# Optimization experiments

Hardware: AMD Instinct MI355X
Metric: run time of the kernel (lower is better)

Reference implementation:

```python
import jax, jax.numpy as jnp
import numpy as np

N = 8192
IN_F = 256
HID = 192
OUT_F = 3


def setup_inputs() -> dict:
    key = jax.random.key(0)
    ks = jax.random.split(key, 8)
    features = jax.random.normal(ks[0], (N, IN_F), dtype=jnp.float32)
    # dense (row-stochastic-ish) adjacency; sparse pattern scaled to keep magnitudes sane
    adj = (jax.random.uniform(ks[1], (N, N), dtype=jnp.float32) < (32.0 / N)).astype(jnp.float32) / 32.0
    def winit(k, shape):
        stdv = 0.6 * 6.0 / np.sqrt(shape[0] + shape[1])
        return jax.random.uniform(k, shape, jnp.float32, -stdv, stdv)
    W1 = winit(ks[2], (IN_F, HID))
    b1 = jax.random.uniform(ks[3], (HID,), jnp.float32, -0.1, 0.1)
    W_mid = jnp.stack([winit(jax.random.fold_in(ks[4], i), (HID, HID)) for i in range(12)])
    b_mid = jax.random.uniform(ks[5], (12, HID), jnp.float32, -0.1, 0.1)
    W_out = winit(ks[6], (HID, OUT_F))
    b_out = jax.random.uniform(ks[7], (OUT_F,), jnp.float32, -0.1, 0.1)
    return dict(features=features, adj=adj, W1=W1, b1=b1,
                W_mid=W_mid, b_mid=b_mid, W_out=W_out, b_out=b_out)


def zngcn(x, adj, W, b):
    # support = x @ W; first side_len cols aggregated over adj, rest passed through
    support = x @ W
    side_len = max(W.shape[1] // 3, 2)
    side_1 = adj @ support[:, :side_len]   # [N, side_len]
    out = jnp.concatenate([side_1, support[:, side_len:]], axis=1)
    return out + b


def reference(features, adj, W1, b1, W_mid, b_mid, W_out, b_out):
    relu = jax.nn.relu
    x = relu(zngcn(features, adj, W1, b1))            # gc1
    x = relu(zngcn(x, adj, W_mid[0], b_mid[0]))       # gc2
    feat = (features[:, :HID] + x) * 0.5
    # gc3..gc12 as 5 residual pairs (W_mid indices 1..10)
    for i in (1, 3, 5, 7, 9):
        x = relu(zngcn(feat, adj, W_mid[i], b_mid[i]))
        x = relu(zngcn(x, adj, W_mid[i + 1], b_mid[i + 1]))
        feat = (feat + x) * 0.5
    # gc13 single layer (W_mid index 11)
    x = relu(zngcn(feat, adj, W_mid[11], b_mid[11]))
    feat = (feat + x) * 0.5
    coords = zngcn(feat, adj, W_out, b_out)           # gc14
    return coords, feat
```

## Files before the change

### kernel.cpp

```cpp
#include <hip/hip_runtime.h>
#include <hip/hip_bf16.h>

#define N_NODES 8192
#define CAP 128
#define XSTR 200
#define FFSTR 193
#define NBLK 512
#define SUPSZ (N_NODES * 64)
#define LEAF_BASE 16384

typedef short s16x8 __attribute__((ext_vector_type(8)));
typedef float f32x4 __attribute__((ext_vector_type(4)));
typedef unsigned short u16x8 __attribute__((ext_vector_type(8)));

__device__ __forceinline__ void cstoref(float* p, float v) {
    __hip_atomic_store(p, v, __ATOMIC_RELAXED, __HIP_MEMORY_SCOPE_AGENT);
}
__device__ __forceinline__ void cstoreh(unsigned short* p, unsigned short v) {
    __hip_atomic_store(p, v, __ATOMIC_RELAXED, __HIP_MEMORY_SCOPE_AGENT);
}
__device__ __forceinline__ void cstorei(int* p, int v) {
    __hip_atomic_store(p, v, __ATOMIC_RELAXED, __HIP_MEMORY_SCOPE_AGENT);
}
__device__ __forceinline__ int cloadi(const int* p) {
    return __hip_atomic_load(p, __ATOMIC_RELAXED, __HIP_MEMORY_SCOPE_AGENT);
}
__device__ __forceinline__ float b2f(unsigned short u) {
    union { unsigned int i; float f; } c; c.i = ((unsigned int)u) << 16; return c.f;
}
__device__ __forceinline__ unsigned short f2b(float f) {
    return __bfloat16_as_ushort(__float2bfloat16(f));
}

__global__ __launch_bounds__(256) void prep(
    const unsigned int* __restrict__ adj,
    const float* __restrict__ W1, const float* __restrict__ Wm,
    int* __restrict__ cnt, int* __restrict__ cols,
    unsigned short* __restrict__ Wt1, unsigned short* __restrict__ WtM)
{
    const int tid = threadIdx.x;
    if (blockIdx.x >= 2048) {
        int idx = (int)(blockIdx.x - 2048) * 256 + tid;
        if (idx >= 6144 + 55296) return;
        const float* src; unsigned short* dst; int KT, t, c, lane;
        if (idx < 6144) {
            KT = 8; src = W1; dst = Wt1;
            t = idx / 512; c = (idx >> 6) & 7; lane = idx & 63;
        } else {
            int r = idx - 6144;
            int mat = r / 4608;
            int rem = r % 4608;
            KT = 6; src = Wm + (size_t)mat * 36864; dst = WtM + (size_t)mat * 36864;
            t = rem / 384; c = (rem >> 6) % 6; lane = rem & 63;
        }
        int n = t * 16 + (lane & 15);
        int k0 = c * 32 + ((lane >> 4) << 3);
        u16x8 o;
#pragma unroll
        for (int j = 0; j < 8; ++j)
            o[j] = f2b(src[(size_t)(k0 + j) * 192 + n]);
        *reinterpret_cast<u16x8*>(dst + ((size_t)(t * KT + c) * 64 + lane) * 8) = o;
        return;
    }

    __shared__ int cntL[4];
    __shared__ int colsL[4][CAP];
    const int wave = tid >> 6;
    const int lane = tid & 63;
    const int row = (int)blockIdx.x * 4 + wave;
    if (lane == 0) cntL[wave] = 0;
    __syncthreads();

    const unsigned int* arow = adj + ((size_t)row << 13);
    uint4 buf[2][8];
    auto loadb = [&](int b, uint4* v) {
#pragma unroll
        for (int i = 0; i < 8; ++i) {
            int chunk = (b * 8 + i) * 64 + lane;
            v[i] = *reinterpret_cast<const uint4*>(arow + ((size_t)chunk << 2));
        }
    };
    loadb(0, buf[0]);
    for (int b = 0; b < 4; ++b) {
        if (b < 3) loadb(b + 1, buf[(b + 1) & 1]);
        uint4* v = buf[b & 1];
#pragma unroll
        for (int i = 0; i < 8; ++i) {
            if ((v[i].x | v[i].y | v[i].z | v[i].w) == 0u) continue;
            int e0 = ((b * 8 + i) * 64 + lane) << 2;
            int loc[4]; int k = 0;
            if (v[i].x) loc[k++] = e0;
            if (v[i].y) loc[k++] = e0 + 1;
            if (v[i].z) loc[k++] = e0 + 2;
            if (v[i].w) loc[k++] = e0 + 3;
            int pos = atomicAdd(&cntL[wave], k);
            for (int j = 0; j < k; ++j)
                if (pos + j < CAP) colsL[wave][pos + j] = loc[j];
        }
    }
    __syncthreads();
    int n = cntL[wave]; if (n > CAP) n = CAP;
    if (lane == 0) cnt[row] = n;
    for (int j = lane; j < CAP; j += 64)
        cols[(size_t)row * CAP + j] = (j < n) ? colsL[wave][j] : 0;
}

__device__ __forceinline__ void gbar_arrive(int* bar, int phase) {
    asm volatile("s_waitcnt vmcnt(0)" ::: "memory");
    __syncthreads();
    if (threadIdx.x == 0)
        cstorei(bar + blockIdx.x * 32, phase);
}
__device__ __forceinline__ void gbar_wait(int* bar, int phase) {
    const int tid = threadIdx.x;
    if (tid < 64) {
        if ((blockIdx.x & 15) == 0) {
            const int leaf = blockIdx.x >> 4;
            int rounds = 0;
            for (;;) {
                int v = (tid < 16) ? cloadi(bar + (leaf * 16 + tid) * 32)
                                   : 0x7fffffff;
#pragma unroll
                for (int off = 32; off > 0; off >>= 1)
                    v = min(v, __shfl_xor(v, off));
                if (v >= phase) break;
                __builtin_amdgcn_s_sleep(1);
                if (++rounds > (1 << 20)) break;
            }
            if (tid == 0) cstorei(bar + LEAF_BASE + leaf * 32, phase);
        }
        int rounds = 0;
        for (;;) {
            int v = (tid < 32) ? cloadi(bar + LEAF_BASE + tid * 32)
                               : 0x7fffffff;
#pragma unroll
            for (int off = 32; off > 0; off >>= 1)
                v = min(v, __shfl_xor(v, off));
            if (v >= phase) break;
            if (rounds < 8) __builtin_amdgcn_s_sleep(1);
            else            __builtin_amdgcn_s_sleep(4);
            if (++rounds > (1 << 20)) break;
        }
    }
    __syncthreads();
}

template<int KT>
__device__ __forceinline__ void load_a(s16x8* a, const unsigned short* xs,
                                       int lane, int quad) {
    const short* xr = reinterpret_cast<const short*>(xs) + (lane & 15) * XSTR + quad * 8;
#pragma unroll
    for (int c = 0; c < KT; ++c) a[c] = *reinterpret_cast<const s16x8*>(xr + c * 32);
}

__device__ __forceinline__ void load_a_feat(s16x8* a, const float* __restrict__ features,
                                            int m0, int lane, int quad) {
    const float* fr = features + (((size_t)(m0 + (lane & 15))) << 8) + quad * 8;
#pragma unroll
    for (int c = 0; c < 8; ++c) {
        float4 f0 = *reinterpret_cast<const float4*>(fr + c * 32);
        float4 f1 = *reinterpret_cast<const float4*>(fr + c * 32 + 4);
        s16x8 v;
        v[0] = (short)f2b(f0.x); v[1] = (short)f2b(f0.y);
        v[2] = (short)f2b(f0.z); v[3] = (short)f2b(f0.w);
        v[4] = (short)f2b(f1.x); v[5] = (short)f2b(f1.y);
        v[6] = (short)f2b(f1.z); v[7] = (short)f2b(f1.w);
        a[c] = v;
    }
}

template<int EP>
__device__ __forceinline__ void pass_epilogue(
    const f32x4& acc, int n, const float* __restrict__ bias,
    unsigned short* xdst, float* featL,
    const float* __restrict__ featG, float* __restrict__ outFeat,
    int m0, int quad)
{
#pragma unroll
    for (int r = 0; r < 4; ++r) {
        const int m = quad * 4 + r;
        float v = acc[r] + bias[n];
        float x = fmaxf(v, 0.f);
        if constexpr (EP == 0) {
            xdst[m * XSTR + n] = f2b(x);
        } else if constexpr (EP == 1) {
            float f = (featG[(size_t)(m0 + m) * 256 + n] + x) * 0.5f;
            featL[m * FFSTR + n] = f;
            xdst[m * XSTR + n] = f2b(f);
        } else if constexpr (EP == 2) {
            float f = (featL[m * FFSTR + n] + x) * 0.5f;
            featL[m * FFSTR + n] = f;
            xdst[m * XSTR + n] = f2b(f);
        } else {
            float f = (featL[m * FFSTR + n] + x) * 0.5f;
            featL[m * FFSTR + n] = f;
            outFeat[(size_t)(m0 + m) * 192 + n] = f;
        }
    }
}

template<int EP>
__device__ __forceinline__ void agg_phase(
    const unsigned short* __restrict__ supR,
    const int* colsL, const int* cntL,
    const float* __restrict__ bias, unsigned short* xdst,
    float* featL, const float* __restrict__ featG,
    float* __restrict__ outFeat,
    int m0, int lane, int wave)
{
    const int base = wave * 4;
    int na[4];
#pragma unroll
    for (int rr = 0; rr < 4; ++rr) na[rr] = cntL[base + rr];
    int nmax = max(max(na[0], na[1]), max(na[2], na[3]));
    float s[4] = {0.f, 0.f, 0.f, 0.f};
    for (int k = 0; k < nmax; k += 8) {
        float v[32];
#pragma unroll
        for (int rr = 0; rr < 4; ++rr) {
            int4 c0 = *reinterpret_cast<const int4*>(colsL + (base + rr) * CAP + k);
            int4 c1 = *reinterpret_cast<const int4*>(colsL + (base + rr) * CAP + k + 4);
            v[rr * 8 + 0] = b2f(supR[((size_t)(c0.x & 8191) << 6) + lane]);
            v[rr * 8 + 1] = b2f(supR[((size_t)(c0.y & 8191) << 6) + lane]);
            v[rr * 8 + 2] = b2f(supR[((size_t)(c0.z & 8191) << 6) + lane]);
            v[rr * 8 + 3] = b2f(supR[((size_t)(c0.w & 8191) << 6) + lane]);
            v[rr * 8 + 4] = b2f(supR[((size_t)(c1.x & 8191) << 6) + lane]);
            v[rr * 8 + 5] = b2f(supR[((size_t)(c1.y & 8191) << 6) + lane]);
            v[rr * 8 + 6] = b2f(supR[((size_t)(c1.z & 8191) << 6) + lane]);
            v[rr * 8 + 7] = b2f(supR[((size_t)(c1.w & 8191) << 6) + lane]);
        }
#pragma unroll
        for (int rr = 0; rr < 4; ++rr) {
#pragma unroll
            for (int j = 0; j < 8; ++j)
                s[rr] += (k + j < na[rr]) ? v[rr * 8 + j] : 0.f;
        }
    }
#pragma unroll
    for (int rr = 0; rr < 4; ++rr) {
        const int lrow = base + rr;
        const int row = m0 + lrow;
        float vv = s[rr] * 0.03125f + bias[lane];
        float x = fmaxf(vv, 0.f);
        if constexpr (EP == 0) {
            xdst[lrow * XSTR + lane] = f2b(x);
        } else if constexpr (EP == 1) {
            float f = (featG[(size_t)row * 256 + lane] + x) * 0.5f;
            featL[lrow * FFSTR + lane] = f;
            xdst[lrow * XSTR + lane] = f2b(f);
        } else if constexpr (EP == 2) {
            float f = (featL[lrow * FFSTR + lane] + x) * 0.5f;
            featL[lrow * FFSTR + lane] = f;
            xdst[lrow * XSTR + lane] = f2b(f);
        } else {
            float f = (featL[lrow * FFSTR + lane] + x) * 0.5f;
            featL[lrow * FFSTR + lane] = f;
            outFeat[(size_t)row * 192 + lane] = f;
        }
    }
}

template<int EPprev, int EPcur>
__device__ __forceinline__ void layer_step(
    int* bar, int ph,
    unsigned short* xsPrev, unsigned short* xsCur,
    const unsigned short* __restrict__ supPrev, unsigned short* __restrict__ supCur,
    const unsigned short* __restrict__ Wt,
    const float* __restrict__ biasPrev, const float* __restrict__ biasCur,
    float* featL, const float* __restrict__ featG, float* __restrict__ outFeat,
    const int* colsL, const int* cntL,
    int m0, int lane, int wave, int quad)
{
    gbar_wait(bar, ph);
    agg_phase<EPprev>(supPrev, colsL, cntL, biasPrev, xsPrev, featL, featG,
                      outFeat, m0, lane, wave);
    __syncthreads();
    s16x8 a[6];
    load_a<6>(a, xsPrev, lane, quad);
    const short* wb = reinterpret_cast<const short*>(Wt);
    {
        f32x4 accS = {};
        const short* wp = wb + ((size_t)wave * 6 * 64 + lane) * 8;
#pragma unroll
        for (int c = 0; c < 6; ++c) {
            s16x8 b = *reinterpret_cast<const s16x8*>(wp + (size_t)c * 512);
            accS = __builtin_amdgcn_mfma_f32_16x16x32_bf16(a[c], b, accS, 0, 0, 0);
        }
        const int n = wave * 16 + (lane & 15);
#pragma unroll
        for (int r = 0; r < 4; ++r)
            cstoreh(&supCur[(((size_t)(m0 + quad * 4 + r)) << 6) + n], f2b(accS[r]));
    }
    gbar_arrive(bar, ph + 1);
#pragma unroll
    for (int p = 0; p < 2; ++p) {
        const int t = 4 + p * 4 + wave;
        f32x4 acc = {};
        const short* wp = wb + ((size_t)t * 6 * 64 + lane) * 8;
#pragma unroll
        for (int c = 0; c < 6; ++c) {
            s16x8 b = *reinterpret_cast<const s16x8*>(wp + (size_t)c * 512);
            acc = __builtin_amdgcn_mfma_f32_16x16x32_bf16(a[c], b, acc, 0, 0, 0);
        }
        const int n = t * 16 + (lane & 15);
        pass_epilogue<EPcur>(acc, n, biasCur, xsCur, featL, featG, outFeat, m0, quad);
    }
}

__global__ __launch_bounds__(256, 2) void fused_layers(
    const float* __restrict__ features,
    const int* __restrict__ cnt, const int* __restrict__ cols,
    const unsigned short* __restrict__ Wt1, const unsigned short* __restrict__ WtM,
    const float* __restrict__ b1, const float* __restrict__ bm,
    const float* __restrict__ Wout, const float* __restrict__ bout,
    unsigned short* __restrict__ supBase, float* __restrict__ sup3,
    float* __restrict__ out, float* __restrict__ outFeat,
    int* __restrict__ bar)
{
    __shared__ unsigned short xsA[16 * XSTR];
    __shared__ unsigned short xsB[16 * XSTR];
    __shared__ float featL[16 * FFSTR];
    __shared__ int colsL[16 * CAP];
    __shared__ int cntL[16];

    const int tid = threadIdx.x;
    const int lane = tid & 63;
    const int wave = tid >> 6;
    const int quad = lane >> 4;
    const int m0 = blockIdx.x * 16;

    {
        s16x8 a8[8];
        load_a_feat(a8, features, m0, lane, quad);
        const short* wb = reinterpret_cast<const short*>(Wt1);
        {
            f32x4 accS = {};
            const short* wp = wb + ((size_t)wave * 8 * 64 + lane) * 8;
#pragma unroll
            for (int c = 0; c < 8; ++c) {
                s16x8 b = *reinterpret_cast<const s16x8*>(wp + (size_t)c * 512);
                accS = __builtin_amdgcn_mfma_f32_16x16x32_bf16(a8[c], b, accS, 0, 0, 0);
            }
            const int n = wave * 16 + (lane & 15);
#pragma unroll
            for (int r = 0; r < 4; ++r)
                cstoreh(&supBase[(((size_t)(m0 + quad * 4 + r)) << 6) + n], f2b(accS[r]));
        }
        gbar_arrive(bar, 1);
#pragma unroll
        for (int p = 0; p < 2; ++p) {
            const int t = 4 + p * 4 + wave;
            f32x4 acc = {};
            const short* wp = wb + ((size_t)t * 8 * 64 + lane) * 8;
#pragma unroll
            for (int c = 0; c < 8; ++c) {
                s16x8 b = *reinterpret_cast<const s16x8*>(wp + (size_t)c * 512);
                acc = __builtin_amdgcn_mfma_f32_16x16x32_bf16(a8[c], b, acc, 0, 0, 0);
            }
            const int n = t * 16 + (lane & 15);
            pass_epilogue<0>(acc, n, b1, xsA, featL, features, outFeat, m0, quad);
        }
    }
    for (int i = tid; i < 16 * (CAP / 4); i += 256) {
        int r = i >> 5;
        int g = (i & 31) << 2;
        *reinterpret_cast<int4*>(&colsL[r * CAP + g]) =
            *reinterpret_cast<const int4*>(cols + (size_t)(m0 + r) * CAP + g);
    }
    if (tid < 16) {
        int nn = cnt[m0 + tid];
        cntL[tid] = nn > CAP ? CAP : nn;
    }

    int ph = 1;
    layer_step<0, 1>(bar, ph, xsA, xsB, supBase, supBase + SUPSZ,
                     WtM, b1, bm, featL, features, outFeat,
                     colsL, cntL, m0, lane, wave, quad);
    ++ph;
    layer_step<1, 0>(bar, ph, xsB, xsA, supBase + SUPSZ, supBase + 2 * SUPSZ,
                     WtM + 36864, bm, bm + 192, featL, features, outFeat,
                     colsL, cntL, m0, lane, wave, quad);
    ++ph;
    layer_step<0, 2>(bar, ph, xsA, xsB, supBase + 2 * SUPSZ, supBase + 3 * SUPSZ,
                     WtM + 2 * 36864, bm + 192, bm + 2 * 192, featL, features,
                     outFeat, colsL, cntL, m0, lane, wave, quad);
    ++ph;

    for (int p = 1; p <= 4; ++p) {
        const int l = 3 + 2 * p;
        layer_step<2, 0>(bar, ph, xsB, xsA,
                         supBase + (size_t)(l - 2) * SUPSZ,
                         supBase + (size_t)(l - 1) * SUPSZ,
                         WtM + (size_t)(l - 2) * 36864,
                         bm + (l - 3) * 192, bm + (l - 2) * 192,
                         featL, features, outFeat, colsL, cntL,
                         m0, lane, wave, quad);
        ++ph;
        const int l2 = l + 1;
        layer_step<0, 2>(bar, ph, xsA, xsB,
                         supBase + (size_t)(l2 - 2) * SUPSZ,
                         supBase + (size_t)(l2 - 1) * SUPSZ,
                         WtM + (size_t)(l2 - 2) * 36864,
                         bm + (l2 - 3) * 192, bm + (l2 - 2) * 192,
                         featL, features, outFeat, colsL, cntL,
                         m0, lane, wave, quad);
        ++ph;
    }

    layer_step<2, 3>(bar, ph, xsB, xsA, supBase + 11 * SUPSZ, supBase + 12 * SUPSZ,
                     WtM + 11 * 36864, bm + 10 * 192, bm + 11 * 192,
                     featL, features, outFeat, colsL, cntL, m0, lane, wave, quad);
    ++ph;

    __syncthreads();
    float s3[4][3];
#pragma unroll
    for (int rr = 0; rr < 4; ++rr) { s3[rr][0] = 0.f; s3[rr][1] = 0.f; s3[rr][2] = 0.f; }
#pragma unroll
    for (int rr = 0; rr < 4; ++rr) {
        const int lrow = wave * 4 + rr;
#pragma unroll
        for (int pp = 1; pp < 3; ++pp) {
            int kk = pp * 64 + lane;
            float f = featL[lrow * FFSTR + kk];
            s3[rr][0] += f * Wout[kk * 3 + 0];
            s3[rr][1] += f * Wout[kk * 3 + 1];
            s3[rr][2] += f * Wout[kk * 3 + 2];
        }
    }
    gbar_wait(bar, ph);
    agg_phase<3>(supBase + (size_t)12 * SUPSZ, colsL, cntL, bm + 11 * 192,
                 xsA, featL, features, outFeat, m0, lane, wave);
    __syncthreads();
#pragma unroll
    for (int rr = 0; rr < 4; ++rr) {
        const int lrow = wave * 4 + rr;
        float f = featL[lrow * FFSTR + lane];
        float s0 = s3[rr][0] + f * Wout[lane * 3 + 0];
        float s1 = s3[rr][1] + f * Wout[lane * 3 + 1];
        float s2 = s3[rr][2] + f * Wout[lane * 3 + 2];
#pragma unroll
        for (int off = 32; off > 0; off >>= 1) {
            s0 += __shfl_down(s0, off);
            s1 += __shfl_down(s1, off);
            s2 += __shfl_down(s2, off);
        }
        if (lane == 0) {
            float* sp = sup3 + (((size_t)(m0 + lrow)) << 2);
            cstoref(sp + 0, s0);
            cstoref(sp + 1, s1);
            cstoref(sp + 2, s2);
        }
    }
    gbar_arrive(bar, ++ph);
    gbar_wait(bar, ph);

    {
        const int lrow = tid >> 4;
        const int row = m0 + lrow;
        const int sub = tid & 15;
        int n = cntL[lrow];
        const int* cl = colsL + lrow * CAP;
        float s0 = 0.f, s1 = 0.f;
        for (int k = sub; k < n; k += 16) {
            int j = cl[k];
            s0 += sup3[((size_t)j << 2) + 0];
            s1 += sup3[((size_t)j << 2) + 1];
        }
#pragma unroll
        for (int off = 8; off > 0; off >>= 1) {
            s0 += __shfl_down(s0, off, 16);
            s1 += __shfl_down(s1, off, 16);
        }
        if (sub == 0) {
            float* op = out + (size_t)row * 3;
            op[0] = s0 * 0.03125f + bout[0];
            op[1] = s1 * 0.03125f + bout[1];
            op[2] = sup3[((size_t)row << 2) + 2] + bout[2];
        }
    }
}

extern "C" void kernel_launch(void* const* d_in, const int* in_sizes, int n_in,
                              void* d_out, int out_size, void* d_ws, size_t ws_size,
                              hipStream_t stream) {
    const float* features = (const float*)d_in[0];
    const unsigned int* adj = (const unsigned int*)d_in[1];
    const float* W1 = (const float*)d_in[2];
    const float* b1 = (const float*)d_in[3];
    const float* Wm = (const float*)d_in[4];
    const float* bm = (const float*)d_in[5];
    const float* Wo = (const float*)d_in[6];
    const float* bo = (const float*)d_in[7];
    float* out = (float*)d_out;
    float* outFeat = out + (size_t)N_NODES * 3;

    char* w = (char*)d_ws;
    int* bar = (int*)(w);
    int* cnt = (int*)(w + 131072);
    int* cols = (int*)(w + 163840);
    unsigned short* supBase = (unsigned short*)(w + 4358144);
    float* sup3 = (float*)(w + 17989632);
    unsigned short* Wt1 = (unsigned short*)(w + 18120704);
    unsigned short* WtM = (unsigned short*)(w + 18219008);

    hipMemsetAsync(bar, 0, 131072, stream);
    prep<<<2288, 256, 0, stream>>>(adj, W1, Wm, cnt, cols, Wt1, WtM);
    fused_layers<<<NBLK, 256, 0, stream>>>(features, cnt, cols, Wt1, WtM, b1, bm,
                                           Wo, bo, supBase, sup3, out, outFeat, bar);

    (void)in_sizes; (void)n_in; (void)out_size; (void)ws_size;
}
```

Before: 585.5 us.

## Fuse adjacency compaction and weight transform into persistent layer kernel

Removes the separate prep kernel. Each persistent block now transforms a slice of the weights, scans its own 16 adjacency rows directly into shared-memory neighbor lists, and then passes a global barrier before the first layer. This drops a launch, the global cnt/cols round trip and the kernel boundary. The cost is that only 512 blocks (2 per CU) must stream the 256MB adjacency matrix instead of 2048 blocks, which may lower memory-level parallelism, and it adds an extra grid barrier phase.

Measured after the change: 586.0 us. No clear change (+0.1%).

```diff
diff --git a/kernel.cpp b/kernel.cpp
--- a/kernel.cpp
+++ b/kernel.cpp
@@ -30,79 +30,6 @@
 }
 __device__ __forceinline__ unsigned short f2b(float f) {
     return __bfloat16_as_ushort(__float2bfloat16(f));
-}
-
-__global__ __launch_bounds__(256) void prep(
-    const unsigned int* __restrict__ adj,
-    const float* __restrict__ W1, const float* __restrict__ Wm,
-    int* __restrict__ cnt, int* __restrict__ cols,
-    unsigned short* __restrict__ Wt1, unsigned short* __restrict__ WtM)
-{
-    const int tid = threadIdx.x;
-    if (blockIdx.x >= 2048) {
-        int idx = (int)(blockIdx.x - 2048) * 256 + tid;
-        if (idx >= 6144 + 55296) return;
-        const float* src; unsigned short* dst; int KT, t, c, lane;
-        if (idx < 6144) {
-            KT = 8; src = W1; dst = Wt1;
-            t = idx / 512; c = (idx >> 6) & 7; lane = idx & 63;
-        } else {
-            int r = idx - 6144;
-            int mat = r / 4608;
-            int rem = r % 4608;
-            KT = 6; src = Wm + (size_t)mat * 36864; dst = WtM + (size_t)mat * 36864;
-            t = rem / 384; c = (rem >> 6) % 6; lane = rem & 63;
-        }
-        int n = t * 16 + (lane & 15);
-        int k0 = c * 32 + ((lane >> 4) << 3);
-        u16x8 o;
-#pragma unroll
-        for (int j = 0; j < 8; ++j)
-            o[j] = f2b(src[(size_t)(k0 + j) * 192 + n]);
-        *reinterpret_cast<u16x8*>(dst + ((size_t)(t * KT + c) * 64 + lane) * 8) = o;
-        return;
-    }
-
-    __shared__ int cntL[4];
-    __shared__ int colsL[4][CAP];
-    const int wave = tid >> 6;
-    const int lane = tid & 63;
-    const int row = (int)blockIdx.x * 4 + wave;
-    if (lane == 0) cntL[wave] = 0;
-    __syncthreads();
-
-    const unsigned int* arow = adj + ((size_t)row << 13);
-    uint4 buf[2][8];
-    auto loadb = [&](int b, uint4* v) {
-#pragma unroll
-        for (int i = 0; i < 8; ++i) {
-            int chunk = (b * 8 + i) * 64 + lane;
-            v[i] = *reinterpret_cast<const uint4*>(arow + ((size_t)chunk << 2));
-        }
-    };
-    loadb(0, buf[0]);
-    for (int b = 0; b < 4; ++b) {
-        if (b < 3) loadb(b + 1, buf[(b + 1) & 1]);
-        uint4* v = buf[b & 1];
-#pragma unroll
-        for (int i = 0; i < 8; ++i) {
-            if ((v[i].x | v[i].y | v[i].z | v[i].w) == 0u) continue;
-            int e0 = ((b * 8 + i) * 64 + lane) << 2;
-            int loc[4]; int k = 0;
-            if (v[i].x) loc[k++] = e0;
-            if (v[i].y) loc[k++] = e0 + 1;
-            if (v[i].z) loc[k++] = e0 + 2;
-            if (v[i].w) loc[k++] = e0 + 3;
-            int pos = atomicAdd(&cntL[wave], k);
-            for (int j = 0; j < k; ++j)
-                if (pos + j < CAP) colsL[wave][pos + j] = loc[j];
-        }
-    }
-    __syncthreads();
-    int n = cntL[wave]; if (n > CAP) n = CAP;
-    if (lane == 0) cnt[row] = n;
-    for (int j = lane; j < CAP; j += 64)
-        cols[(size_t)row * CAP + j] = (j < n) ? colsL[wave][j] : 0;
 }
 
 __device__ __forceinline__ void gbar_arrive(int* bar, int phase) {
@@ -143,6 +70,34 @@
         }
     }
     __syncthreads();
+}
+
+__device__ __forceinline__ void transform_slice(int idx,
+    const float* __restrict__ W1, const float* __restrict__ Wm,
+    unsigned short* __restrict__ Wt1, unsigned short* __restrict__ WtM)
+{
+    if (idx >= 6144 + 55296) return;
+    const float* src; unsigned short* dst; int KT, t, c, lane;
+    if (idx < 6144) {
+        KT = 8; src = W1; dst = Wt1;
+        t = idx / 512; c = (idx >> 6) & 7; lane = idx & 63;
+    } else {
+        int r = idx - 6144;
+        int mat = r / 4608;
+        int rem = r % 4608;
+        KT = 6; src = Wm + (size_t)mat * 36864; dst = WtM + (size_t)mat * 36864;
+        t = rem / 384; c = (rem >> 6) % 6; lane = rem & 63;
+    }
+    int n = t * 16 + (lane & 15);
+    int k0 = c * 32 + ((lane >> 4) << 3);
+    union { u16x8 v; unsigned long long q[2]; } u;
+#pragma unroll
+    for (int j = 0; j < 8; ++j)
+        u.v[j] = f2b(src[(size_t)(k0 + j) * 192 + n]);
+    unsigned long long* dp =
+        (unsigned long long*)(dst + ((size_t)(t * KT + c) * 64 + lane) * 8);
+    __hip_atomic_store(dp,     u.q[0], __ATOMIC_RELAXED, __HIP_MEMORY_SCOPE_AGENT);
+    __hip_atomic_store(dp + 1, u.q[1], __ATOMIC_RELAXED, __HIP_MEMORY_SCOPE_AGENT);
 }
 
 template<int KT>
@@ -307,10 +262,11 @@
     }
 }
 
-__global__ __launch_bounds__(256, 2) void fused_layers(
+__global__ __launch_bounds__(256, 2) void fused_gcn(
     const float* __restrict__ features,
-    const int* __restrict__ cnt, const int* __restrict__ cols,
-    const unsigned short* __restrict__ Wt1, const unsigned short* __restrict__ WtM,
+    const unsigned int* __restrict__ adj,
+    const float* __restrict__ W1, const float* __restrict__ Wm,
+    unsigned short* __restrict__ Wt1, unsigned short* __restrict__ WtM,
     const float* __restrict__ b1, const float* __restrict__ bm,
     const float* __restrict__ Wout, const float* __restrict__ bout,
     unsigned short* __restrict__ supBase, float* __restrict__ sup3,
@@ -329,6 +285,46 @@
     const int quad = lane >> 4;
     const int m0 = blockIdx.x * 16;
 
+    if (tid < 16) cntL[tid] = 0;
+    transform_slice(blockIdx.x * 256 + tid, W1, Wm, Wt1, WtM);
+    gbar_arrive(bar, 1);
+
+    {
+        uint4 buf[2][8];
+        auto loadb = [&](int t, uint4* v) {
+            const unsigned int* arow =
+                adj + ((size_t)(m0 + wave * 4 + (t >> 2)) << 13);
+            const int b = t & 3;
+#pragma unroll
+            for (int i = 0; i < 8; ++i) {
+                int g = b * 512 + i * 64 + lane;
+                v[i] = *reinterpret_cast<const uint4*>(arow + ((size_t)g << 2));
+            }
+        };
+        loadb(0, buf[0]);
+        for (int t = 0; t < 16; ++t) {
+            if (t < 15) loadb(t + 1, buf[(t + 1) & 1]);
+            uint4* v = buf[t & 1];
+            const int r = wave * 4 + (t >> 2);
+#pragma unroll
+            for (int i = 0; i < 8; ++i) {
+                if ((v[i].x | v[i].y | v[i].z | v[i].w) == 0u) continue;
+                int e0 = ((t & 3) * 512 + i * 64 + lane) << 2;
+                int loc[4]; int k = 0;
+                if (v[i].x) loc[k++] = e0;
+                if (v[i].y) loc[k++] = e0 + 1;
+                if (v[i].z) loc[k++] = e0 + 2;
+                if (v[i].w) loc[k++] = e0 + 3;
+                int pos = atomicAdd(&cntL[r], k);
+                for (int j = 0; j < k; ++j)
+                    if (pos + j < CAP) colsL[r * CAP + pos + j] = loc[j];
+            }
+        }
+    }
+    __syncthreads();
+    if (tid < 16) cntL[tid] = cntL[tid] > CAP ? CAP : cntL[tid];
+    gbar_wait(bar, 1);
+
     {
         s16x8 a8[8];
         load_a_feat(a8, features, m0, lane, quad);
@@ -346,7 +342,7 @@
             for (int r = 0; r < 4; ++r)
                 cstoreh(&supBase[(((size_t)(m0 + quad * 4 + r)) << 6) + n], f2b(accS[r]));
         }
-        gbar_arrive(bar, 1);
+        gbar_arrive(bar, 2);
 #pragma unroll
         for (int p = 0; p < 2; ++p) {
             const int t = 4 + p * 4 + wave;
@@ -361,18 +357,8 @@
             pass_epilogue<0>(acc, n, b1, xsA, featL, features, outFeat, m0, quad);
         }
     }
-    for (int i = tid; i < 16 * (CAP / 4); i += 256) {
-        int r = i >> 5;
-        int g = (i & 31) << 2;
-        *reinterpret_cast<int4*>(&colsL[r * CAP + g]) =
-            *reinterpret_cast<const int4*>(cols + (size_t)(m0 + r) * CAP + g);
-    }
-    if (tid < 16) {
-        int nn = cnt[m0 + tid];
-        cntL[tid] = nn > CAP ? CAP : nn;
-    }
-
-    int ph = 1;
+
+    int ph = 2;
     layer_step<0, 1>(bar, ph, xsA, xsB, supBase, supBase + SUPSZ,
                      WtM, b1, bm, featL, features, outFeat,
                      colsL, cntL, m0, lane, wave, quad);
@@ -497,17 +483,14 @@
 
     char* w = (char*)d_ws;
     int* bar = (int*)(w);
-    int* cnt = (int*)(w + 131072);
-    int* cols = (int*)(w + 163840);
-    unsigned short* supBase = (unsigned short*)(w + 4358144);
-    float* sup3 = (float*)(w + 17989632);
-    unsigned short* Wt1 = (unsigned short*)(w + 18120704);
-    unsigned short* WtM = (unsigned short*)(w + 18219008);
+    unsigned short* supBase = (unsigned short*)(w + 131072);
+    float* sup3 = (float*)(w + 13762560);
+    unsigned short* Wt1 = (unsigned short*)(w + 13893632);
+    unsigned short* WtM = (unsigned short*)(w + 13991936);
 
     hipMemsetAsync(bar, 0, 131072, stream);
-    prep<<<2288, 256, 0, stream>>>(adj, W1, Wm, cnt, cols, Wt1, WtM);
-    fused_layers<<<NBLK, 256, 0, stream>>>(features, cnt, cols, Wt1, WtM, b1, bm,
-                                           Wo, bo, supBase, sup3, out, outFeat, bar);
+    fused_gcn<<<NBLK, 256, 0, stream>>>(features, adj, W1, Wm, Wt1, WtM, b1, bm,
+                                        Wo, bo, supBase, sup3, out, outFeat, bar);
 
     (void)in_sizes; (void)n_in; (void)out_size; (void)ws_size;
 }
```
